# Kernel tuning notes

Hardware: AMD Instinct MI355X
Metric: run time of the kernel (lower is better)

Reference implementation:

```python
import jax, jax.numpy as jnp
import numpy as np

N_NODES = 64
NUM_STEPS = 15
N_DP = 5
SLOPE = 25.0  # fast_sigmoid surrogate slope


def _spike(x):
    # forward Heaviside; surrogate grad only matters in bwd module
    return (x > 0).astype(x.dtype)


def _lif(x, mem, beta, thr):
    # snnTorch Leaky, reset_mechanism='subtract': reset from previous mem (detached)
    reset = jax.lax.stop_gradient((mem > thr).astype(x.dtype))
    mem = beta * mem + x - reset * thr
    spk = _spike(mem - thr)
    return spk, mem


def setup_inputs() -> dict:
    key = jax.random.key(0)
    ks = jax.random.split(key, 16)
    B = 2048
    def xavier(k, shape):
        fan_in, fan_out = shape
        lim = float(np.sqrt(6.0 / (fan_in + fan_out)))
        return jax.random.uniform(k, shape, jnp.float32, -lim, lim)
    return {
        "L_norm": jax.random.normal(ks[0], (B, N_NODES, N_NODES), jnp.float32),
        "X_seq": jax.random.normal(ks[1], (B, NUM_STEPS, N_NODES, 1), jnp.float32),
        "W_proj": xavier(ks[2], (1, 16)),   "b_proj": jnp.zeros((16,), jnp.float32),
        "W_gcn1": xavier(ks[3], (16, 32)),  "b_gcn1": jnp.zeros((32,), jnp.float32),
        "W_skip1": xavier(ks[4], (16, 32)), "b_skip1": jnp.zeros((32,), jnp.float32),
        "W_gcn2": xavier(ks[5], (32, 64)),  "b_gcn2": jnp.zeros((64,), jnp.float32),
        "W_skip2": xavier(ks[6], (32, 64)), "b_skip2": jnp.zeros((64,), jnp.float32),
        "W_c1": xavier(ks[7], (N_NODES * 64, 128)), "b_c1": jnp.zeros((128,), jnp.float32),
        "W_c2": xavier(ks[8], (128, 4)),    "b_c2": jnp.zeros((4,), jnp.float32),
    }


def reference(L_norm, X_seq, W_proj, b_proj, W_gcn1, b_gcn1, W_skip1, b_skip1,
              W_gcn2, b_gcn2, W_skip2, b_skip2, W_c1, b_c1, W_c2, b_c2):
    B = X_seq.shape[0]

    def hr_gcn(x, mems, Wg, bg, Ws, bs, betas, thrs):
        # dense Laplacian conv: (L @ (x W)) + b, plus triple LIF + linear skip
        cur = jnp.einsum("bnm,bmf->bnf", L_norm, x @ Wg) + bg
        spk_a, m_a = _lif(cur, mems[0], betas[0], thrs[0])
        spk_n, m_n = _lif(cur, mems[1], betas[1], thrs[1])
        spk_m, m_m = _lif(cur, mems[2], betas[2], thrs[2])
        spk_out = spk_a + spk_n + spk_m + (x @ Ws + bs)
        return spk_out, (m_a, m_n, m_m)

    z = lambda f: jnp.zeros((B, N_NODES, f), jnp.float32)
    carry0 = ((z(32),) * 3, (z(64),) * 3, z(64))

    def step(carry, x_t):
        mems1, mems2, mem_li = carry
        x = x_t @ W_proj + b_proj                      # [B, N, 16]
        spk1, mems1 = hr_gcn(x, mems1, W_gcn1, b_gcn1, W_skip1, b_skip1,
                             (0.8, 0.9, 0.95), (0.8, 1.0, 1.5))
        spk2, mems2 = hr_gcn(spk1, mems2, W_gcn2, b_gcn2, W_skip2, b_skip2,
                             (0.8, 0.9, 0.95), (0.8, 1.0, 1.5))
        mem_li = 0.9 * mem_li + spk2                   # Leaky, reset 'none'
        pot = mem_li.reshape(B, -1)                    # [B, N*64]
        return (mems1, mems2, mem_li), pot

    xs = jnp.swapaxes(X_seq, 0, 1)                     # [T, B, N, 1]
    _, pots = jax.lax.scan(step, carry0, xs)
    potentials = jnp.swapaxes(pots, 0, 1)              # [B, T, N*64]

    # DP decoder (dropout = identity in eval)
    dp_feat = potentials[:, -N_DP:, :].mean(axis=1) - potentials[:, :N_DP, :].mean(axis=1)
    h = jax.nn.relu(dp_feat @ W_c1 + b_c1)
    return h @ W_c2 + b_c2
```

## Files before the change

### kernel.cpp

```cpp
#include <hip/hip_runtime.h>
#include <hip/hip_bf16.h>


typedef __attribute__((ext_vector_type(8))) short s16x8;
typedef __attribute__((ext_vector_type(4))) float f32x4;
#define MFMA16(a, b, c) __builtin_amdgcn_mfma_f32_16x16x32_bf16(a, b, c, 0, 0, 0)

__device__ __forceinline__ short f2bs(float x) {
  union { __hip_bfloat16 h; short s; } u; u.h = __float2bfloat16(x); return u.s;
}
__device__ __forceinline__ float bs2f(short s) {
  union { short s; __hip_bfloat16 h; } u; u.s = s; return __bfloat162float(u.h);
}

#define LIF_STEP(mem, beta, thr, cur, spksum)                \
  {                                                          \
    float r_ = ((mem) > (thr)) ? (thr) : 0.0f;               \
    (mem) = (beta) * (mem) + (cur) - r_;                     \
    (spksum) += (((mem) - (thr)) > 0.0f) ? 1.0f : 0.0f;      \
  }

#define LFS 68
#define RS  36

__global__ __launch_bounds__(512, 2)
void hrsnn_main(const float* __restrict__ Lg,  const float* __restrict__ Xg,
                const float* __restrict__ Wp,  const float* __restrict__ bp,
                const float* __restrict__ Wg1, const float* __restrict__ bg1,
                const float* __restrict__ Ws1, const float* __restrict__ bs1,
                const float* __restrict__ Wg2, const float* __restrict__ bg2,
                const float* __restrict__ Ws2, const float* __restrict__ bs2,
                unsigned int* __restrict__ dp_out)
{
  __shared__ __align__(16) float UBUF[4608];
  float* const Lf    = UBUF;
  float* const S1row = UBUF;
  float* const Mrow  = UBUF + 2304;
  __shared__ __align__(16) short WgF[4 * 3 * 64 * 8];
  __shared__ __align__(16) unsigned int XtHL[960];
  __shared__ __align__(16) float Xtf[960];
  __shared__ float LxS[64], LsumS[64];
  __shared__ float u1A[32], cb1A[32], us1v[32], cs1v[32];
  __shared__ float u2gA[64], c2gA[64], u2sA[64], cs2A[64];

  const int tid = threadIdx.x;
  const int b = blockIdx.x;
  const int l = tid & 63, w = tid >> 6;
  const int p = w >> 1, h = w & 1;
  const int q = l >> 4, c = l & 15;
  const int R = 16 * p;

  const float* Lb = Lg + (size_t)b * 4096;
#pragma unroll
  for (int k = 0; k < 2; k++) {
    const int i4 = tid + 512 * k;
    const float4 v = *(const float4*)&Lb[i4 * 4];
    *(float4*)&Lf[(i4 >> 4) * LFS + (i4 & 15) * 4] = v;
  }
  const float* Xb = Xg + (size_t)b * 960;
  for (int i = tid; i < 960; i += 512) {
    const float x = Xb[i];
    const short hs = f2bs(x);
    const short ls = f2bs(x - bs2f(hs));
    XtHL[i] = ((unsigned int)(unsigned short)hs << 16) | (unsigned short)ls;
    Xtf[i] = x;
  }
  if (tid < 32) {
    const int f = tid;
    float a = 0.f, bb = 0.f, cc = 0.f, d = 0.f;
    for (int k = 0; k < 16; k++) {
      const float wp = Wp[k], bpv = bp[k];
      const float wg = Wg1[k * 32 + f], ws = Ws1[k * 32 + f];
      a += wp * wg; bb += bpv * wg;
      cc += wp * ws; d += bpv * ws;
    }
    u1A[f] = a; cb1A[f] = bb;
    us1v[f] = cc; cs1v[f] = d + bs1[f];
  }
  __syncthreads();

  {
    const int n = tid >> 3, o = tid & 7;
    const float4 a4 = *(const float4*)&Lf[n * LFS + 8 * o];
    const float4 b4 = *(const float4*)&Lf[n * LFS + 8 * o + 4];
    float ps = a4.x + a4.y + a4.z + a4.w + b4.x + b4.y + b4.z + b4.w;
    ps += __shfl_xor(ps, 1, 64);
    ps += __shfl_xor(ps, 2, 64);
    ps += __shfl_xor(ps, 4, 64);
    if (o == 0) LsumS[n] = ps;
  }
  s16x8 Lh[2], Lm[2], Ll[2];
#pragma unroll
  for (int s = 0; s < 2; s++) {
    const float* rp = &Lf[(R + c) * LFS + 32 * s + 8 * q];
    const float4 v0 = *(const float4*)rp;
    const float4 v1 = *(const float4*)(rp + 4);
    float v[8] = {v0.x, v0.y, v0.z, v0.w, v1.x, v1.y, v1.z, v1.w};
#pragma unroll
    for (int j = 0; j < 8; j++) {
      const short hh = f2bs(v[j]);       const float r1 = v[j] - bs2f(hh);
      const short mm = f2bs(r1);         const float r2 = r1 - bs2f(mm);
      Lh[s][j] = hh; Lm[s][j] = mm; Ll[s][j] = f2bs(r2);
    }
  }
  {
    const int tt = w & 3;
    float v[8];
#pragma unroll
    for (int j = 0; j < 8; j++) v[j] = Wg2[(8 * q + j) * 64 + 16 * tt + c];
    if (w < 4) {
      s16x8 fh, fm;
#pragma unroll
      for (int j = 0; j < 8; j++) {
        const short hh = f2bs(v[j]);
        fh[j] = hh; fm[j] = f2bs(v[j] - bs2f(hh));
      }
      *(s16x8*)&WgF[((tt * 3 + 0) * 64 + l) * 8] = fh;
      *(s16x8*)&WgF[((tt * 3 + 1) * 64 + l) * 8] = fm;
    } else {
      s16x8 fl;
#pragma unroll
      for (int j = 0; j < 8; j++) {
        const short hh = f2bs(v[j]);     const float r1 = v[j] - bs2f(hh);
        const short mm = f2bs(r1);       const float r2 = r1 - bs2f(mm);
        fl[j] = f2bs(r2);
      }
      *(s16x8*)&WgF[((tt * 3 + 2) * 64 + l) * 8] = fl;
    }
  }
  s16x8 WsH[2], WsL[2];
#pragma unroll
  for (int i = 0; i < 2; i++) {
    const int g0 = 32 * h + 16 * i;
#pragma unroll
    for (int j = 0; j < 8; j++) {
      const float x = Ws2[(8 * q + j) * 64 + g0 + c];
      const short hh = f2bs(x);
      WsH[i][j] = hh; WsL[i][j] = f2bs(x - bs2f(hh));
    }
  }
  __syncthreads();

  if (tid < 64) {
    const int g = tid;
    float a = 0.f, bb = 0.f, cc = 0.f, d = 0.f;
    for (int f = 0; f < 32; f++) {
      const float wg = Wg2[f * 64 + g], ws = Ws2[f * 64 + g];
      a += us1v[f] * wg; bb += cs1v[f] * wg;
      cc += us1v[f] * ws; d += cs1v[f] * ws;
    }
    u2gA[g] = a; c2gA[g] = bb; u2sA[g] = cc; cs2A[g] = d + bs2[g];
  }
  __syncthreads();

  float u2g2[2], u2s2[2], cs22[2], c2c[2][4];
#pragma unroll
  for (int i = 0; i < 2; i++) {
    const int g = 32 * h + 16 * i + c;
    u2g2[i] = u2gA[g]; u2s2[i] = u2sA[g]; cs22[i] = cs2A[g];
    const float cg = c2gA[g], bg = bg2[g];
#pragma unroll
    for (int r = 0; r < 4; r++) c2c[i][r] = LsumS[R + 4 * q + r] * cg + bg;
  }
  const int f1 = tid & 31, nb = tid >> 5;
  const float u1f = u1A[f1];
  float k1c[4];
  {
    const float cb = cb1A[f1], bg = bg1[f1];
#pragma unroll
    for (int j = 0; j < 4; j++) k1c[j] = LsumS[nb + 16 * j] * cb + bg;
  }

  float m1a[4], m1n[4], m1m[4];
#pragma unroll
  for (int j = 0; j < 4; j++) { m1a[j] = 0.f; m1n[j] = 0.f; m1m[j] = 0.f; }
  float m2a[2][4], m2n[2][4], m2m[2][4], mli[2][4], dpa[2][4];
#pragma unroll
  for (int i = 0; i < 2; i++)
#pragma unroll
    for (int r = 0; r < 4; r++) {
      m2a[i][r] = 0.f; m2n[i][r] = 0.f; m2m[i][r] = 0.f;
      mli[i][r] = 0.f; dpa[i][r] = 0.f;
    }

  const f32x4 fz = {0.f, 0.f, 0.f, 0.f};
  __syncthreads();

  for (int t = 0; t < 15; t++) {
    f32x4 lx = fz;
#pragma unroll
    for (int s = 0; s < 2; s++) {
      const unsigned int* xw = &XtHL[t * 64 + 32 * s + 8 * q];
      const uint4 w0 = *(const uint4*)xw;
      const uint4 w1 = *(const uint4*)(xw + 4);
      unsigned int wv[8] = {w0.x, w0.y, w0.z, w0.w, w1.x, w1.y, w1.z, w1.w};
      s16x8 bh, bl;
#pragma unroll
      for (int j = 0; j < 8; j++) {
        bh[j] = (short)(wv[j] >> 16);
        bl[j] = (short)(wv[j] & 0xffff);
      }
      lx = MFMA16(Lh[s], bh, lx);
      lx = MFMA16(Lm[s], bh, lx);
      lx = MFMA16(Lh[s], bl, lx);
    }
    if (h == 0 && c == 0) {
#pragma unroll
      for (int r = 0; r < 4; r++) LxS[R + 4 * q + r] = lx[r];
    }
    __syncthreads();

#pragma unroll
    for (int j = 0; j < 4; j++) {
      const int n = nb + 16 * j;
      const float cur = LxS[n] * u1f + k1c[j];
      float ss = 0.f;
      LIF_STEP(m1a[j], 0.8f, 0.8f, cur, ss);
      LIF_STEP(m1n[j], 0.9f, 1.0f, cur, ss);
      LIF_STEP(m1m[j], 0.95f, 1.5f, cur, ss);
      S1row[n * RS + f1] = ss;
    }
    __syncthreads();

    f32x4 macc = fz;
#pragma unroll
    for (int s = 0; s < 2; s++) {
      s16x8 bS;
#pragma unroll
      for (int j = 0; j < 8; j++)
        bS[j] = f2bs(S1row[(32 * s + 8 * q + j) * RS + 16 * h + c]);
      macc = MFMA16(Lh[s], bS, macc);
      macc = MFMA16(Lm[s], bS, macc);
      macc = MFMA16(Ll[s], bS, macc);
    }
#pragma unroll
    for (int r = 0; r < 4; r++) Mrow[(R + 4 * q + r) * RS + 16 * h + c] = macc[r];

    f32x4 sacc[2];
    {
      const float* rp = &S1row[(R + c) * RS + 8 * q];
      const float4 v0 = *(const float4*)rp;
      const float4 v1 = *(const float4*)(rp + 4);
      const float v[8] = {v0.x, v0.y, v0.z, v0.w, v1.x, v1.y, v1.z, v1.w};
      s16x8 aS;
#pragma unroll
      for (int j = 0; j < 8; j++) aS[j] = f2bs(v[j]);
#pragma unroll
      for (int i = 0; i < 2; i++) {
        sacc[i] = MFMA16(aS, WsH[i], fz);
        sacc[i] = MFMA16(aS, WsL[i], sacc[i]);
      }
    }
    __syncthreads();

    s16x8 aMh, aMm, aMl;
    {
      const float* rp = &Mrow[(R + c) * RS + 8 * q];
      const float4 v0 = *(const float4*)rp;
      const float4 v1 = *(const float4*)(rp + 4);
      const float v[8] = {v0.x, v0.y, v0.z, v0.w, v1.x, v1.y, v1.z, v1.w};
#pragma unroll
      for (int j = 0; j < 8; j++) {
        const short hh = f2bs(v[j]);     const float r1 = v[j] - bs2f(hh);
        const short mm = f2bs(r1);       const float r2 = r1 - bs2f(mm);
        aMh[j] = hh; aMm[j] = mm; aMl[j] = f2bs(r2);
      }
    }
    float xtn[4];
#pragma unroll
    for (int r = 0; r < 4; r++) xtn[r] = Xtf[t * 64 + R + 4 * q + r];

#pragma unroll
    for (int i = 0; i < 2; i++) {
      const int tt = 2 * h + i;
      const s16x8 bGh = *(const s16x8*)&WgF[((tt * 3 + 0) * 64 + l) * 8];
      const s16x8 bGm = *(const s16x8*)&WgF[((tt * 3 + 1) * 64 + l) * 8];
      const s16x8 bGl = *(const s16x8*)&WgF[((tt * 3 + 2) * 64 + l) * 8];
      f32x4 cacc = fz;
      cacc = MFMA16(aMh, bGh, cacc);
      cacc = MFMA16(aMh, bGm, cacc);
      cacc = MFMA16(aMm, bGh, cacc);
      cacc = MFMA16(aMh, bGl, cacc);
      cacc = MFMA16(aMm, bGm, cacc);
      cacc = MFMA16(aMl, bGh, cacc);
#pragma unroll
      for (int r = 0; r < 4; r++) {
        const float cur2 = cacc[r] + lx[r] * u2g2[i] + c2c[i][r];
        float ss = 0.f;
        LIF_STEP(m2a[i][r], 0.8f, 0.8f, cur2, ss);
        LIF_STEP(m2n[i][r], 0.9f, 1.0f, cur2, ss);
        LIF_STEP(m2m[i][r], 0.95f, 1.5f, cur2, ss);
        const float spk2 = ss + sacc[i][r] + xtn[r] * u2s2[i] + cs22[i];
        mli[i][r] = 0.9f * mli[i][r] + spk2;
      }
    }
    if (t < 5) {
#pragma unroll
      for (int i = 0; i < 2; i++)
#pragma unroll
        for (int r = 0; r < 4; r++) dpa[i][r] -= mli[i][r];
    } else if (t >= 10) {
#pragma unroll
      for (int i = 0; i < 2; i++)
#pragma unroll
        for (int r = 0; r < 4; r++) dpa[i][r] += mli[i][r];
    }
  }

  unsigned int* dpb = dp_out + (size_t)b * 4096;
#pragma unroll
  for (int i = 0; i < 2; i++) {
    const int g = 32 * h + 16 * i + c;
#pragma unroll
    for (int r = 0; r < 4; r++) {
      const int n = R + 4 * q + r;
      const float v = dpa[i][r] * 0.2f;
      const short hh = f2bs(v);
      const short ll = f2bs(v - bs2f(hh));
      dpb[n * 64 + g] = ((unsigned int)(unsigned short)hh << 16) | (unsigned short)ll;
    }
  }
}

__global__ __launch_bounds__(512, 1)
void hrsnn_decoder(const unsigned int* __restrict__ dpq, const float* __restrict__ W1,
                   const float* __restrict__ b1, const float* __restrict__ W2,
                   const float* __restrict__ b2, float* __restrict__ out)
{
  __shared__ __align__(16) float H[16][132];
  const int tid = threadIdx.x;
  const int l = tid & 63, tt = tid >> 6;
  const int q = l >> 4, c = l & 15;

  const unsigned int* arow = dpq + (size_t)(blockIdx.x * 16 + c) * 4096 + 8 * q;
  const float* bcol = W1 + (8 * q) * 128 + 16 * tt + c;

  f32x4 acc = {0.f, 0.f, 0.f, 0.f};
  for (int s = 0; s < 128; s++) {
    const uint4 a0 = *(const uint4*)(arow + 32 * s);
    const uint4 a1 = *(const uint4*)(arow + 32 * s + 4);
    const unsigned int av[8] = {a0.x, a0.y, a0.z, a0.w, a1.x, a1.y, a1.z, a1.w};
    s16x8 Ah, Al, Bh, Bl;
#pragma unroll
    for (int j = 0; j < 8; j++) {
      Ah[j] = (short)(av[j] >> 16);
      Al[j] = (short)(av[j] & 0xffff);
      const float x = bcol[(32 * s + j) * 128];
      const short hh = f2bs(x);
      Bh[j] = hh; Bl[j] = f2bs(x - bs2f(hh));
    }
    acc = MFMA16(Ah, Bh, acc);
    acc = MFMA16(Al, Bh, acc);
    acc = MFMA16(Ah, Bl, acc);
  }

  const float bk = b1[16 * tt + c];
#pragma unroll
  for (int r = 0; r < 4; r++) {
    const float hv = acc[r] + bk;
    H[4 * q + r][16 * tt + c] = hv > 0.f ? hv : 0.f;
  }
  __syncthreads();

  if (tid < 64) {
    const int i = tid >> 2, o = tid & 3;
    float s = b2[o];
    for (int k = 0; k < 128; k++) s += H[i][k] * W2[k * 4 + o];
    out[(size_t)(blockIdx.x * 16 + i) * 4 + o] = s;
  }
}

extern "C" void kernel_launch(void* const* d_in, const int* in_sizes, int n_in,
                              void* d_out, int out_size, void* d_ws, size_t ws_size,
                              hipStream_t stream)
{
  const float* Lg  = (const float*)d_in[0];
  const float* Xg  = (const float*)d_in[1];
  const float* Wp  = (const float*)d_in[2];
  const float* bp  = (const float*)d_in[3];
  const float* Wg1 = (const float*)d_in[4];
  const float* bg1 = (const float*)d_in[5];
  const float* Ws1 = (const float*)d_in[6];
  const float* bs1 = (const float*)d_in[7];
  const float* Wg2 = (const float*)d_in[8];
  const float* bg2 = (const float*)d_in[9];
  const float* Ws2 = (const float*)d_in[10];
  const float* bs2 = (const float*)d_in[11];
  const float* W1  = (const float*)d_in[12];
  const float* b1  = (const float*)d_in[13];
  const float* W2  = (const float*)d_in[14];
  const float* b2  = (const float*)d_in[15];

  unsigned int* dpq = (unsigned int*)d_ws;
  float* out = (float*)d_out;

  hipLaunchKernelGGL(hrsnn_main, dim3(2048), dim3(512), 0, stream,
                     Lg, Xg, Wp, bp, Wg1, bg1, Ws1, bs1, Wg2, bg2, Ws2, bs2, dpq);
  hipLaunchKernelGGL(hrsnn_decoder, dim3(128), dim3(512), 0, stream,
                     dpq, W1, b1, W2, b2, out);
}
```

Measured before the change: 473.8 us.

## Split decoder across two blocks per batch tile with atomic output and prefetch

The decoder grid doubles to 256 blocks of 256 threads, with each block computing half of the 128 hidden columns. The two halves are combined through atomicAdd into an output zeroed by a memset, and each half contributes half of b2. A-operand loads are software-prefetched two steps ahead to overlap memory latency with the MFMAs. The main kernel's launch bound is raised from 2 to 4 blocks per CU, which may force register spilling. The change adds a memset launch and makes the output summation order nondeterministic.

```diff
diff --git a/kernel.cpp b/kernel.cpp
--- a/kernel.cpp
+++ b/kernel.cpp
@@ -23,7 +23,7 @@
 #define LFS 68
 #define RS  36
 
-__global__ __launch_bounds__(512, 2)
+__global__ __launch_bounds__(512, 4)
 void hrsnn_main(const float* __restrict__ Lg,  const float* __restrict__ Xg,
                 const float* __restrict__ Wp,  const float* __restrict__ bp,
                 const float* __restrict__ Wg1, const float* __restrict__ bg1,
@@ -322,51 +322,75 @@
   }
 }
 
-__global__ __launch_bounds__(512, 1)
+
+#define DEC_STEP(S, CA0, CA1)                                          \
+  {                                                                    \
+    const unsigned int av[8] = {(CA0).x, (CA0).y, (CA0).z, (CA0).w,    \
+                                (CA1).x, (CA1).y, (CA1).z, (CA1).w};   \
+    s16x8 Ah, Al, Bh, Bl;                                              \
+    _Pragma("unroll")                                                  \
+    for (int j = 0; j < 8; j++) {                                      \
+      Ah[j] = (short)(av[j] >> 16);                                    \
+      Al[j] = (short)(av[j] & 0xffff);                                 \
+      const float x = bcol[(32 * (S) + j) * 128];                      \
+      const short hh = f2bs(x);                                        \
+      Bh[j] = hh; Bl[j] = f2bs(x - bs2f(hh));                          \
+    }                                                                  \
+    acc = MFMA16(Ah, Bh, acc);                                         \
+    acc = MFMA16(Al, Bh, acc);                                         \
+    acc = MFMA16(Ah, Bl, acc);                                         \
+  }
+
+__global__ __launch_bounds__(256, 4)
 void hrsnn_decoder(const unsigned int* __restrict__ dpq, const float* __restrict__ W1,
                    const float* __restrict__ b1, const float* __restrict__ W2,
                    const float* __restrict__ b2, float* __restrict__ out)
 {
-  __shared__ __align__(16) float H[16][132];
+  __shared__ __align__(16) float H[16][68];
   const int tid = threadIdx.x;
-  const int l = tid & 63, tt = tid >> 6;
+  const int l = tid & 63, tw = tid >> 6;
+  const int g  = blockIdx.x >> 1;
+  const int hb = blockIdx.x & 1;
   const int q = l >> 4, c = l & 15;
-
-  const unsigned int* arow = dpq + (size_t)(blockIdx.x * 16 + c) * 4096 + 8 * q;
-  const float* bcol = W1 + (8 * q) * 128 + 16 * tt + c;
+  const int col = 64 * hb + 16 * tw + c;
+
+  const unsigned int* arow = dpq + (size_t)(g * 16 + c) * 4096 + 8 * q;
+  const float* bcol = W1 + (8 * q) * 128 + col;
 
   f32x4 acc = {0.f, 0.f, 0.f, 0.f};
-  for (int s = 0; s < 128; s++) {
-    const uint4 a0 = *(const uint4*)(arow + 32 * s);
-    const uint4 a1 = *(const uint4*)(arow + 32 * s + 4);
-    const unsigned int av[8] = {a0.x, a0.y, a0.z, a0.w, a1.x, a1.y, a1.z, a1.w};
-    s16x8 Ah, Al, Bh, Bl;
-#pragma unroll
-    for (int j = 0; j < 8; j++) {
-      Ah[j] = (short)(av[j] >> 16);
-      Al[j] = (short)(av[j] & 0xffff);
-      const float x = bcol[(32 * s + j) * 128];
-      const short hh = f2bs(x);
-      Bh[j] = hh; Bl[j] = f2bs(x - bs2f(hh));
-    }
-    acc = MFMA16(Ah, Bh, acc);
-    acc = MFMA16(Al, Bh, acc);
-    acc = MFMA16(Ah, Bl, acc);
-  }
-
-  const float bk = b1[16 * tt + c];
+  uint4 A00 = *(const uint4*)(arow);
+  uint4 A01 = *(const uint4*)(arow + 4);
+  uint4 A10 = *(const uint4*)(arow + 32);
+  uint4 A11 = *(const uint4*)(arow + 36);
+  for (int s = 0; s < 128; s += 2) {
+    const uint4 c00 = A00, c01 = A01;
+    if (s + 2 < 128) {
+      A00 = *(const uint4*)(arow + 32 * (s + 2));
+      A01 = *(const uint4*)(arow + 32 * (s + 2) + 4);
+    }
+    DEC_STEP(s, c00, c01);
+    const uint4 c10 = A10, c11 = A11;
+    if (s + 3 < 128) {
+      A10 = *(const uint4*)(arow + 32 * (s + 3));
+      A11 = *(const uint4*)(arow + 32 * (s + 3) + 4);
+    }
+    DEC_STEP(s + 1, c10, c11);
+  }
+
+  const float bk = b1[col];
 #pragma unroll
   for (int r = 0; r < 4; r++) {
     const float hv = acc[r] + bk;
-    H[4 * q + r][16 * tt + c] = hv > 0.f ? hv : 0.f;
+    H[4 * q + r][16 * tw + c] = hv > 0.f ? hv : 0.f;
   }
   __syncthreads();
 
   if (tid < 64) {
     const int i = tid >> 2, o = tid & 3;
-    float s = b2[o];
-    for (int k = 0; k < 128; k++) s += H[i][k] * W2[k * 4 + o];
-    out[(size_t)(blockIdx.x * 16 + i) * 4 + o] = s;
+    float s = 0.5f * b2[o];
+    const float* w2 = W2 + (64 * hb) * 4 + o;
+    for (int k = 0; k < 64; k++) s += H[i][k] * w2[k * 4];
+    atomicAdd(&out[(size_t)(g * 16 + i) * 4 + o], s);
   }
 }
 
@@ -396,6 +420,7 @@
 
   hipLaunchKernelGGL(hrsnn_main, dim3(2048), dim3(512), 0, stream,
                      Lg, Xg, Wp, bp, Wg1, bg1, Ws1, bs1, Wg2, bg2, Ws2, bs2, dpq);
-  hipLaunchKernelGGL(hrsnn_decoder, dim3(128), dim3(512), 0, stream,
+  hipMemsetAsync(out, 0, (size_t)2048 * 4 * sizeof(float), stream);
+  hipLaunchKernelGGL(hrsnn_decoder, dim3(256), dim3(256), 0, stream,
                      dpq, W1, b1, W2, b2, out);
 }
```

Measured after the change: 809.5 us. 1.71x slower.

## Fuse decoder MLP into main kernel as per-block GEMV tail

Applied to the files above, without the earlier changes.

Removes the separate decoder kernel and the workspace round-trip by having each batch block compute its DP feature vector in shared memory, then perform the 4096x128 linear layer, ReLU and 128x4 output layer itself. This avoids a second launch and the split-bf16 encode/decode of the intermediate features. In exchange, each block streams all of W1 from cache, so total W1 traffic grows substantially and the block's tail latency increases.

```diff
diff --git a/kernel.cpp b/kernel.cpp
--- a/kernel.cpp
+++ b/kernel.cpp
@@ -30,7 +30,9 @@
                 const float* __restrict__ Ws1, const float* __restrict__ bs1,
                 const float* __restrict__ Wg2, const float* __restrict__ bg2,
                 const float* __restrict__ Ws2, const float* __restrict__ bs2,
-                unsigned int* __restrict__ dp_out)
+                const float* __restrict__ W1,  const float* __restrict__ b1,
+                const float* __restrict__ W2,  const float* __restrict__ b2,
+                float* __restrict__ out)
 {
   __shared__ __align__(16) float UBUF[4608];
   float* const Lf    = UBUF;
@@ -307,66 +309,60 @@
     }
   }
 
-  unsigned int* dpb = dp_out + (size_t)b * 4096;
+  __syncthreads();
+  float* const dpS = UBUF;
 #pragma unroll
   for (int i = 0; i < 2; i++) {
     const int g = 32 * h + 16 * i + c;
 #pragma unroll
     for (int r = 0; r < 4; r++) {
       const int n = R + 4 * q + r;
-      const float v = dpa[i][r] * 0.2f;
-      const short hh = f2bs(v);
-      const short ll = f2bs(v - bs2f(hh));
-      dpb[n * 64 + g] = ((unsigned int)(unsigned short)hh << 16) | (unsigned short)ll;
-    }
-  }
-}
-
-__global__ __launch_bounds__(512, 1)
-void hrsnn_decoder(const unsigned int* __restrict__ dpq, const float* __restrict__ W1,
-                   const float* __restrict__ b1, const float* __restrict__ W2,
-                   const float* __restrict__ b2, float* __restrict__ out)
-{
-  __shared__ __align__(16) float H[16][132];
-  const int tid = threadIdx.x;
-  const int l = tid & 63, tt = tid >> 6;
-  const int q = l >> 4, c = l & 15;
-
-  const unsigned int* arow = dpq + (size_t)(blockIdx.x * 16 + c) * 4096 + 8 * q;
-  const float* bcol = W1 + (8 * q) * 128 + 16 * tt + c;
-
-  f32x4 acc = {0.f, 0.f, 0.f, 0.f};
-  for (int s = 0; s < 128; s++) {
-    const uint4 a0 = *(const uint4*)(arow + 32 * s);
-    const uint4 a1 = *(const uint4*)(arow + 32 * s + 4);
-    const unsigned int av[8] = {a0.x, a0.y, a0.z, a0.w, a1.x, a1.y, a1.z, a1.w};
-    s16x8 Ah, Al, Bh, Bl;
-#pragma unroll
-    for (int j = 0; j < 8; j++) {
-      Ah[j] = (short)(av[j] >> 16);
-      Al[j] = (short)(av[j] & 0xffff);
-      const float x = bcol[(32 * s + j) * 128];
-      const short hh = f2bs(x);
-      Bh[j] = hh; Bl[j] = f2bs(x - bs2f(hh));
-    }
-    acc = MFMA16(Ah, Bh, acc);
-    acc = MFMA16(Al, Bh, acc);
-    acc = MFMA16(Ah, Bl, acc);
-  }
-
-  const float bk = b1[16 * tt + c];
-#pragma unroll
-  for (int r = 0; r < 4; r++) {
-    const float hv = acc[r] + bk;
-    H[4 * q + r][16 * tt + c] = hv > 0.f ? hv : 0.f;
-  }
-  __syncthreads();
-
+      dpS[n * 64 + g] = dpa[i][r] * 0.2f;
+    }
+  }
+  __syncthreads();
+
+  const int cg = tid & 31, ks = tid >> 5;
+  float hp0 = 0.f, hp1 = 0.f, hp2 = 0.f, hp3 = 0.f;
+  const float* w1p = W1 + (size_t)(ks * 256) * 128 + 4 * cg;
+  const float* dps = dpS + ks * 256;
+#pragma unroll 4
+  for (int kk = 0; kk < 256; kk++) {
+    const float dv = dps[kk];
+    const float4 wv = *(const float4*)(w1p + (size_t)kk * 128);
+    hp0 += dv * wv.x; hp1 += dv * wv.y;
+    hp2 += dv * wv.z; hp3 += dv * wv.w;
+  }
+  __syncthreads();
+  float* const ph = UBUF;
+  ph[ks * 128 + 4 * cg + 0] = hp0;
+  ph[ks * 128 + 4 * cg + 1] = hp1;
+  ph[ks * 128 + 4 * cg + 2] = hp2;
+  ph[ks * 128 + 4 * cg + 3] = hp3;
+  __syncthreads();
+  float* const hS = UBUF + 2048;
+  if (tid < 128) {
+    float s = b1[tid];
+    for (int k2 = 0; k2 < 16; k2++) s += ph[k2 * 128 + tid];
+    hS[tid] = s > 0.f ? s : 0.f;
+  }
+  __syncthreads();
+  float* const pr = UBUF + 2048 + 128;
   if (tid < 64) {
-    const int i = tid >> 2, o = tid & 3;
-    float s = b2[o];
-    for (int k = 0; k < 128; k++) s += H[i][k] * W2[k * 4 + o];
-    out[(size_t)(blockIdx.x * 16 + i) * 4 + o] = s;
+    const int o = tid & 3, kg = tid >> 2;
+    float s = 0.f;
+#pragma unroll
+    for (int u = 0; u < 8; u++) {
+      const int k2 = kg * 8 + u;
+      s += hS[k2] * W2[k2 * 4 + o];
+    }
+    pr[kg * 4 + o] = s;
+  }
+  __syncthreads();
+  if (tid < 4) {
+    float s = b2[tid];
+    for (int k2 = 0; k2 < 16; k2++) s += pr[k2 * 4 + tid];
+    out[(size_t)b * 4 + tid] = s;
   }
 }
 
@@ -391,11 +387,10 @@
   const float* W2  = (const float*)d_in[14];
   const float* b2  = (const float*)d_in[15];
 
-  unsigned int* dpq = (unsigned int*)d_ws;
   float* out = (float*)d_out;
+  (void)d_ws; (void)ws_size;
 
   hipLaunchKernelGGL(hrsnn_main, dim3(2048), dim3(512), 0, stream,
-                     Lg, Xg, Wp, bp, Wg1, bg1, Ws1, bs1, Wg2, bg2, Ws2, bs2, dpq);
-  hipLaunchKernelGGL(hrsnn_decoder, dim3(128), dim3(512), 0, stream,
-                     dpq, W1, b1, W2, b2, out);
+                     Lg, Xg, Wp, bp, Wg1, bg1, Ws1, bs1, Wg2, bg2, Ws2, bs2,
+                     W1, b1, W2, b2, out);
 }
```

After: 540.3 us. 1.14x slower.
